# Kernel optimization log

Measured on AMD Instinct MI355X. Metric: run time of the kernel, lower is better.

Reference implementation:

```python
import jax, jax.numpy as jnp
import numpy as np
from jax import lax

B, N, C = 4, 4096, 512
NUM_HEADS = 8
HD = C // NUM_HEADS  # 64, equals L
L = 64               # H = W = L, N = L*L


def setup_inputs() -> dict:
    key = jax.random.key(0)
    ks = jax.random.split(key, 8)
    d = HD
    return {
        "x": jax.random.normal(ks[0], (B, N, C), jnp.float32),
        "log_peak_width": jnp.log(jnp.float32(3.0)),
        "log_valley_width": jnp.log(jnp.float32(3.0)),
        "w_qkv": jax.random.normal(ks[1], (3 * C, C), jnp.float32) * 0.02,
        "b_qkv": jnp.zeros((3 * C,), jnp.float32),
        "w_proj": jax.random.normal(ks[2], (C, C), jnp.float32) * 0.02,
        "b_proj": jnp.zeros((C,), jnp.float32),
        "omega": jnp.linspace(0.1, 10.0, d // 2).astype(jnp.float32),
        "w_pp1": jax.random.normal(ks[3], (2 * d, 1, 3), jnp.float32) * 0.3,   # grouped conv, groups=d
        "b_pp1": jnp.zeros((2 * d,), jnp.float32),
        "w_pp2": jax.random.normal(ks[4], (d, 2 * d, 1), jnp.float32) * 0.1,
        "b_pp2": jnp.zeros((d,), jnp.float32),
        "w_gate": jax.random.normal(ks[5], (d, d, 1), jnp.float32) * 0.1,
        "b_gate": jnp.zeros((d,), jnp.float32),
    }


def _spectral_gate(x_spec, log_pw, log_vw):
    # x_spec: [B, C, N]. torch nonzero flattens (b,c,i) -> use per-position counts
    # (exactly equivalent to summing one gaussian per nonzero occurrence).
    n = x_spec.shape[-1]
    sc = jnp.sign(jnp.diff(jnp.diff(x_spec, axis=-1), axis=-1))       # [B,C,N-2]
    peak_cnt = jnp.sum(sc < 0, axis=(0, 1)).astype(x_spec.dtype)      # [N-2]
    valley_cnt = jnp.sum(sc > 0, axis=(0, 1)).astype(x_spec.dtype)    # [N-2]
    pos = jnp.arange(n, dtype=x_spec.dtype)
    centers = jnp.arange(1, n - 1, dtype=x_spec.dtype)                # index i+1

    def gsum(cnt, logw):
        dist = (pos[None, :] - centers[:, None]) * jnp.exp(-logw)     # [N-2, N]
        return cnt @ jnp.exp(-dist * dist)                            # [N]

    attn = gsum(peak_cnt, log_pw) + gsum(valley_cnt, log_vw)
    return (attn - attn.min()) / (attn.max() - attn.min() + 1e-6)     # [N], uniform over (B,C)


def _spectral_pe(omega, w1, b1, w2, b2, wg, bg, l, d):
    grid = jnp.arange(l, dtype=jnp.float32)
    rel = grid[:, None] - grid[None, :]                               # [l,l]
    freqs = rel[..., None] * omega                                    # [l,l,d/2]
    pe = jnp.concatenate([jnp.sin(freqs), jnp.cos(freqs)], axis=-1)   # [l,l,d]
    pe = pe.reshape(l * l, d).T[None]                                 # [1,d,l*l]
    dn = ('NCH', 'OIH', 'NCH')
    h = lax.conv_general_dilated(pe, w1, (1,), [(1, 1)], dimension_numbers=dn,
                                 feature_group_count=d) + b1[None, :, None]
    h = jax.nn.gelu(h, approximate=False)
    pe2 = (lax.conv_general_dilated(h, w2, (1,), [(0, 0)],
                                    dimension_numbers=dn) + b2[None, :, None])[0]  # [d, l*l]
    gate = jax.nn.sigmoid(wg[:, :, 0] @ pe2.mean(-1, keepdims=True) + bg[:, None])  # [d,1]
    pe3 = pe2.T.reshape(l, l, d)
    # torch rearrange '(l1 l2) d -> l1 l2 d' on [d,1] gate: reshape to [l, d//l, 1] and broadcast
    return pe3 * gate.reshape(l, d // l, 1)


def _rope(t, pe, d):
    b, h, n, _ = t.shape
    l = pe.shape[0]
    tr = t.reshape(b, h, l, l, d)
    tr = tr + tr * pe * (d ** -0.25)
    return tr.reshape(b, h, n, d)


def reference(x, log_peak_width, log_valley_width, w_qkv, b_qkv, w_proj, b_proj,
              omega, w_pp1, b_pp1, w_pp2, b_pp2, w_gate, b_gate):
    b, n, c = x.shape
    h, d = NUM_HEADS, HD
    gate = _spectral_gate(x.transpose(0, 2, 1), log_peak_width, log_valley_width)  # [n]
    xg = x * gate[None, :, None]
    qkv = xg @ w_qkv.T + b_qkv                                        # [b,n,3c]
    q, k, v = jnp.split(qkv, 3, axis=-1)
    tohead = lambda t: t.reshape(b, n, h, d).transpose(0, 2, 1, 3)    # [b,h,n,d]
    q, k, v = tohead(q), tohead(k), tohead(v)
    q = jax.nn.elu(q) + 1.0
    k = jax.nn.elu(k) + 1.0
    pe = _spectral_pe(omega, w_pp1, b_pp1, w_pp2, b_pp2, w_gate, b_gate, L, d)
    q = _rope(q, pe, d)
    k = _rope(k, pe, d)
    scale = (d * n) ** -0.5
    ctx = jnp.einsum('bhnd,bhne->bhde', q, k) * scale                 # [b,h,d,d]
    out = jnp.einsum('bhnd,bhde->bhne', v, ctx) * scale               # [b,h,n,d]
    out = out.transpose(0, 2, 1, 3).reshape(b, n, c)
    return out @ w_proj.T + b_proj
```

## Files before the change

### kernel.cpp

```cpp
#include <hip/hip_runtime.h>
#include <hip/hip_bf16.h>
#include <math.h>

constexpr int BB = 4;
constexpr int NN = 4096;
constexpr int CC = 512;
constexpr int HH = 8;
constexpr int DD = 64;
constexpr int NCNT = NN - 2;

typedef __bf16 bf16x8 __attribute__((ext_vector_type(8)));
typedef float f32x4 __attribute__((ext_vector_type(4)));

__device__ __forceinline__ float b2f(ushort u) {
  unsigned v = ((unsigned)u) << 16;
  return __builtin_bit_cast(float, v);
}
__device__ __forceinline__ ushort f2b(float f) {
  __hip_bfloat16 h = __float2bfloat16(f);
  return __builtin_bit_cast(ushort, h);
}
__device__ __forceinline__ void gload16(const ushort* g, ushort* l) {
  __builtin_amdgcn_global_load_lds(
      (const __attribute__((address_space(1))) unsigned int*)g,
      (__attribute__((address_space(3))) unsigned int*)l, 16, 0, 0);
}

__global__ __launch_bounds__(512) void k_front(
    const float* __restrict__ x, int* __restrict__ pcntP,
    int* __restrict__ pcntV, ushort* __restrict__ Xh,
    const float* __restrict__ omega,
    const float* __restrict__ w1, const float* __restrict__ b1,
    const float* __restrict__ w2, const float* __restrict__ b2,
    float* __restrict__ pe2,
    const float* __restrict__ wqkv, ushort* __restrict__ Whqk,
    ushort* __restrict__ Wvth, ushort* __restrict__ Wvtl) {
  __shared__ __attribute__((aligned(16))) char sm[16896];
  const int blk = blockIdx.x;
  const int tid = threadIdx.x;

  if (blk < 1024) {
    int b = blk >> 8;
    int tile = blk & 255;
    int g = tid >> 7;
    int cq = tid & 127;
    int c4 = cq * 4;
    int lane = tid & 63;
    int r0 = tile * 16 + g * 4;
    const float* xb = x + (size_t)b * NN * CC + c4;

    float4 v[6];
    #pragma unroll
    for (int r = 0; r < 6; ++r) {
      int row = r0 + r;
      v[r] = *(const float4*)&xb[(size_t)(row < NN ? row : NN - 1) * CC];
    }

    #pragma unroll
    for (int r = 0; r < 4; ++r) {
      ushort4 h;
      ((ushort*)&h)[0] = f2b(v[r].x);
      ((ushort*)&h)[1] = f2b(v[r].y);
      ((ushort*)&h)[2] = f2b(v[r].z);
      ((ushort*)&h)[3] = f2b(v[r].w);
      *(ushort4*)&Xh[((size_t)b * NN + r0 + r) * CC + c4] = h;
    }

    unsigned* red = (unsigned*)sm;
    if (tid < 16) red[tid] = 0;
    __syncthreads();
    #pragma unroll
    for (int r = 0; r < 4; ++r) {
      int i = r0 + r;
      if (i < NCNT) {
        float d2x = (v[r + 2].x - v[r + 1].x) - (v[r + 1].x - v[r].x);
        float d2y = (v[r + 2].y - v[r + 1].y) - (v[r + 1].y - v[r].y);
        float d2z = (v[r + 2].z - v[r + 1].z) - (v[r + 1].z - v[r].z);
        float d2w = (v[r + 2].w - v[r + 1].w) - (v[r + 1].w - v[r].w);
        unsigned neg = (d2x < 0.f) + (d2y < 0.f) + (d2z < 0.f) + (d2w < 0.f);
        unsigned pos = (d2x > 0.f) + (d2y > 0.f) + (d2z > 0.f) + (d2w > 0.f);
        unsigned packed = neg | (pos << 16);
        #pragma unroll
        for (int off = 32; off > 0; off >>= 1)
          packed += __shfl_down(packed, off);
        if (lane == 0) atomicAdd(&red[g * 4 + r], packed);
      }
    }
    __syncthreads();
    if (tid < 16) {
      int i = tile * 16 + tid;
      unsigned p = red[tid];
      pcntP[b * NN + i] = (i < NCNT) ? (int)(p & 0xffffu) : 0;
      pcntV[b * NN + i] = (i < NCNT) ? (int)(p >> 16) : 0;
    }
  } else if (blk < 1536) {
    int pblk = blk - 1024;
    int g = tid >> 6;
    int j = tid & 63;
    int n = pblk * 8 + g;
    float (*pec)[3][64] = (float (*)[3][64])sm;
    float (*hs)[128] = (float (*)[128])(sm + 6144);
    for (int t = 0; t < 3; ++t) {
      int m = n + t - 1;
      float v = 0.f;
      if (m >= 0 && m < NN) {
        int l1 = m >> 6, l2 = m & 63;
        float rel = (float)(l1 - l2);
        v = (j < 32) ? sinf(rel * omega[j]) : cosf(rel * omega[j - 32]);
      }
      pec[g][t][j] = v;
    }
    __syncthreads();
    for (int o = j; o < 128; o += 64) {
      int ci = o >> 1;
      float hv = b1[o];
      #pragma unroll
      for (int t = 0; t < 3; ++t) hv += pec[g][t][ci] * w1[o * 3 + t];
      hv = 0.5f * hv * (1.f + erff(hv * 0.70710678118654752f));
      hs[g][o] = hv;
    }
    __syncthreads();
    float acc = b2[j];
    for (int o = 0; o < 128; ++o) acc += hs[g][o] * w2[j * 128 + o];
    pe2[(size_t)j * NN + n] = acc;
  } else if (blk < 1792) {
    int hblk = blk - 1536;
    int idx4 = (hblk * 512 + tid) * 4;
    float4 v = *(const float4*)&wqkv[idx4];
    ushort4 h;
    ((ushort*)&h)[0] = f2b(v.x);
    ((ushort*)&h)[1] = f2b(v.y);
    ((ushort*)&h)[2] = f2b(v.z);
    ((ushort*)&h)[3] = f2b(v.w);
    *(ushort4*)&Whqk[idx4] = h;
  } else {
    int wblk = blk - 1792;
    int bx = wblk & 7;
    int by = wblk >> 3;
    float (*t)[65] = (float (*)[65])sm;
    if (tid < 256) {
      #pragma unroll
      for (int it = 0; it < 4; ++it) {
        int idx = tid + it * 256;
        int r = idx >> 4;
        int c4 = (idx & 15) * 4;
        float4 v = *(const float4*)&wqkv[(size_t)(1024 + by * 64 + r) * 512 + bx * 64 + c4];
        t[r][c4] = v.x; t[r][c4 + 1] = v.y; t[r][c4 + 2] = v.z; t[r][c4 + 3] = v.w;
      }
    }
    __syncthreads();
    if (tid < 256) {
      #pragma unroll
      for (int it = 0; it < 4; ++it) {
        int idx = tid + it * 256;
        int r = idx >> 4;
        int c4 = (idx & 15) * 4;
        ushort4 h4, l4;
        #pragma unroll
        for (int q = 0; q < 4; ++q) {
          float v = t[c4 + q][r];
          ushort hi = f2b(v);
          ((ushort*)&h4)[q] = hi;
          ((ushort*)&l4)[q] = f2b(v - b2f(hi));
        }
        size_t o = (size_t)(bx * 64 + r) * 512 + by * 64 + c4;
        *(ushort4*)&Wvth[o] = h4;
        *(ushort4*)&Wvtl[o] = l4;
      }
    }
  }
}

__global__ __launch_bounds__(256) void k_mid1(
    const float* __restrict__ lpw, const float* __restrict__ lvw,
    const int* __restrict__ pcntP, const int* __restrict__ pcntV,
    float* __restrict__ etabP, float* __restrict__ etabV,
    float* __restrict__ fcntP, float* __restrict__ fcntV,
    const float* __restrict__ pe2, const float* __restrict__ wg,
    const float* __restrict__ bg, float* __restrict__ gpe) {
  const int blk = blockIdx.x;
  const int tid = threadIdx.x;
  if (blk < 16) {
    int i = blk * 256 + tid;
    float ipw = expf(-lpw[0]);
    float ivw = expf(-lvw[0]);
    float t1 = (float)i * ipw;
    float t2 = (float)i * ivw;
    etabP[i] = expf(-t1 * t1);
    etabV[i] = expf(-t2 * t2);
    fcntP[i] = (float)(pcntP[i] + pcntP[NN + i] + pcntP[2 * NN + i] + pcntP[3 * NN + i]);
    fcntV[i] = (float)(pcntV[i] + pcntV[NN + i] + pcntV[2 * NN + i] + pcntV[3 * NN + i]);
  } else {
    int j = tid & 63, part = tid >> 6;
    float s = 0.f;
    const float* row = pe2 + (size_t)j * NN + part * 1024;
    for (int t = 0; t < 1024; ++t) s += row[t];
    __shared__ float ps[4][64];
    __shared__ float mean[64];
    ps[part][j] = s;
    __syncthreads();
    if (tid < 64) mean[j] = (ps[0][j] + ps[1][j] + ps[2][j] + ps[3][j]) * (1.f / 4096.f);
    __syncthreads();
    if (tid < 64) {
      float g = bg[j];
      for (int k2 = 0; k2 < 64; ++k2) g += wg[j * 64 + k2] * mean[k2];
      gpe[j] = 1.f / (1.f + expf(-g));
    }
  }
}

__global__ __launch_bounds__(256) void k_mid2(
    const float* __restrict__ fcntP, const float* __restrict__ fcntV,
    const float* __restrict__ etabP, const float* __restrict__ etabV,
    float* __restrict__ attn,
    const float* __restrict__ pe2, const float* __restrict__ gpe,
    float* __restrict__ ropem) {
  const int blk = blockIdx.x;
  const int tid = threadIdx.x;
  if (blk < 4096) {
    int p = blk;
    float acc = 0.f;
    for (int i = tid; i < NCNT; i += 256) {
      int a = p - 1 - i;
      a = a < 0 ? -a : a;
      acc += fcntP[i] * etabP[a] + fcntV[i] * etabV[a];
    }
    __shared__ float red[256];
    red[tid] = acc;
    __syncthreads();
    for (int s = 128; s > 0; s >>= 1) {
      if (tid < s) red[tid] += red[tid + s];
      __syncthreads();
    }
    if (tid == 0) attn[p] = red[0];
  } else {
    int idx = (blk - 4096) * 256 + tid;
    int n = idx >> 6, dd = idx & 63;
    ropem[idx] = 1.f + pe2[(size_t)dd * NN + n] * gpe[n >> 6] * 0.35355339059327373f;
  }
}

__global__ void k_norm(const float* __restrict__ attn, float* __restrict__ gate) {
  int tid = threadIdx.x;
  float v0 = attn[tid], v1 = attn[tid + 1024], v2 = attn[tid + 2048], v3 = attn[tid + 3072];
  float mn = fminf(fminf(v0, v1), fminf(v2, v3));
  float mx = fmaxf(fmaxf(v0, v1), fmaxf(v2, v3));
  __shared__ float rmn[1024], rmx[1024];
  rmn[tid] = mn; rmx[tid] = mx;
  __syncthreads();
  for (int s = 512; s > 0; s >>= 1) {
    if (tid < s) {
      rmn[tid] = fminf(rmn[tid], rmn[tid + s]);
      rmx[tid] = fmaxf(rmx[tid], rmx[tid + s]);
    }
    __syncthreads();
  }
  float lo = rmn[0];
  float denom = rmx[0] - rmn[0] + 1e-6f;
  gate[tid]        = (v0 - lo) / denom;
  gate[tid + 1024] = (v1 - lo) / denom;
  gate[tid + 2048] = (v2 - lo) / denom;
  gate[tid + 3072] = (v3 - lo) / denom;
}

template <int BN, int EPI>
__global__ __launch_bounds__(512) void k_gemm8(
    const ushort* __restrict__ Ag, const ushort* __restrict__ Bgh,
    const float* __restrict__ bias, const float* __restrict__ gate,
    const float* __restrict__ ropem,
    float* __restrict__ outF, ushort* __restrict__ qT, ushort* __restrict__ kT,
    int ntn, int ncols) {
  constexpr int NF = BN / 32;
  constexpr int BCH = BN / 16;
  const int nwg = gridDim.x;
  const int hw = blockIdx.x;
  const int logical = (hw & 7) * (nwg >> 3) + (hw >> 3);
  const int m0 = (logical / ntn) * 256, n0 = (logical % ntn) * BN;

  const int tid = threadIdx.x, wave = tid >> 6, lane = tid & 63;
  const int wm = wave >> 1, wn = wave & 1;
  __shared__ ushort sA[2][8192];
  __shared__ ushort sB[2][BN * 32];
  f32x4 acc[4][NF] = {};

  const int lr = lane >> 2;
  const int ci = lane & 3;
  const int scol = (ci ^ ((lr >> 1) & 3)) * 8;
  const int rA = lane & 15;
  const int cswz = ((lane >> 4) ^ ((rA >> 1) & 3)) * 8;

  const ushort* pA0 = Ag + (size_t)(m0 + (2 * wave) * 16 + lr) * CC + scol;
  const ushort* pA1 = Ag + (size_t)(m0 + (2 * wave + 1) * 16 + lr) * CC + scol;
  const ushort* Bh_ = Bgh + (EPI == 2 ? (size_t)(m0 >> 12) * 262144 : 0);
  const ushort* pB0 = Bh_ + (size_t)(n0 + wave * 16 + lr) * CC + scol;

#define STAGE(T, S)                                                        \
  {                                                                        \
    gload16(pA0 + (T) * 32, &sA[S][(2 * wave) * 512]);                     \
    gload16(pA1 + (T) * 32, &sA[S][(2 * wave + 1) * 512]);                 \
    if (BCH == 8) {                                                        \
      gload16(pB0 + (T) * 32, &sB[S][wave * 512]);                         \
    } else {                                                               \
      if (wave < BCH) gload16(pB0 + (T) * 32, &sB[S][wave * 512]);         \
    }                                                                      \
  }

  STAGE(0, 0);
  __syncthreads();

  #pragma unroll
  for (int t = 0; t < 16; ++t) {
    if (t < 15) STAGE(t + 1, (t + 1) & 1);
    const int cur = t & 1;
    bf16x8 af[4], bhf[NF];
    #pragma unroll
    for (int m = 0; m < 4; ++m)
      af[m] = *(const bf16x8*)(&sA[cur][(wm * 64 + m * 16 + rA) * 32 + cswz]);
    #pragma unroll
    for (int n = 0; n < NF; ++n)
      bhf[n] = *(const bf16x8*)(&sB[cur][(wn * (BN / 2) + n * 16 + rA) * 32 + cswz]);
    #pragma unroll
    for (int m = 0; m < 4; ++m)
      #pragma unroll
      for (int n = 0; n < NF; ++n)
        acc[m][n] = __builtin_amdgcn_mfma_f32_16x16x32_bf16(af[m], bhf[n], acc[m][n], 0, 0, 0);
    __syncthreads();
  }
#undef STAGE

  const int kj = lane >> 4, l15 = lane & 15;
  #pragma unroll
  for (int m = 0; m < 4; ++m) {
    #pragma unroll
    for (int n = 0; n < NF; ++n) {
      if (EPI == 2) {
        #pragma unroll
        for (int r = 0; r < 4; ++r) {
          int row = m0 + wm * 64 + m * 16 + kj * 4 + r;
          int col = n0 + wn * (BN / 2) + n * 16 + l15;
          int nseq = row & (NN - 1), b = row >> 12;
          float val = acc[m][n][r] * gate[nseq] + bias[b * 512 + col];
          outF[(size_t)row * ncols + col] = val;
        }
      } else {
        int rowb = m0 + wm * 64 + m * 16 + kj * 4;
        int col = n0 + wn * (BN / 2) + n * 16 + l15;
        int nseqb = rowb & (NN - 1), b = rowb >> 12;
        int part = col >> 9, h = (col >> 6) & 7, dd = col & 63;
        ushort4 pk;
        #pragma unroll
        for (int r = 0; r < 4; ++r) {
          int nseq = nseqb + r;
          float val = acc[m][n][r] * gate[nseq] + bias[col];
          float e = val > 0.f ? val + 1.f : expf(val);
          ((ushort*)&pk)[r] = f2b(e * ropem[nseq * 64 + dd]);
        }
        ushort* dst = (part == 0 ? qT : kT) +
                      ((size_t)(b * HH + h) * DD + dd) * NN + nseqb;
        *(ushort4*)dst = pk;
      }
    }
  }
}

__global__ __launch_bounds__(256) void k_ctx_mfma(
    const ushort* __restrict__ qT, const ushort* __restrict__ kT,
    float* __restrict__ ctxp) {
  int blk = blockIdx.x;
  int bh = blk >> 4, chunk = blk & 15;
  int wave = threadIdx.x >> 6, lane = threadIdx.x & 63;
  int l15 = lane & 15, kj = lane >> 4;
  const size_t base = (size_t)bh * DD * NN;
  const int n0 = chunk * 256 + wave * 64;
  f32x4 acc[4][4] = {};
  #pragma unroll
  for (int ks = 0; ks < 2; ++ks) {
    const int nb = n0 + ks * 32 + kj * 8;
    bf16x8 qa[4], ka[4];
    #pragma unroll
    for (int m = 0; m < 4; ++m)
      qa[m] = *(const bf16x8*)(qT + base + (size_t)(m * 16 + l15) * NN + nb);
    #pragma unroll
    for (int n = 0; n < 4; ++n)
      ka[n] = *(const bf16x8*)(kT + base + (size_t)(n * 16 + l15) * NN + nb);
    #pragma unroll
    for (int m = 0; m < 4; ++m)
      #pragma unroll
      for (int n = 0; n < 4; ++n)
        acc[m][n] = __builtin_amdgcn_mfma_f32_16x16x32_bf16(qa[m], ka[n], acc[m][n], 0, 0, 0);
  }
  __shared__ float red[4][4096];
  #pragma unroll
  for (int m = 0; m < 4; ++m)
    #pragma unroll
    for (int n = 0; n < 4; ++n)
      #pragma unroll
      for (int r = 0; r < 4; ++r)
        red[wave][(m * 16 + kj * 4 + r) * 64 + n * 16 + l15] = acc[m][n][r];
  __syncthreads();
  const float scale = 1.f / 512.f;
  float* dst = ctxp + (size_t)(bh * 16 + chunk) * 4096;
  #pragma unroll
  for (int e = 0; e < 16; ++e) {
    int idx = threadIdx.x + e * 256;
    float s = red[0][idx] + red[1][idx] + red[2][idx] + red[3][idx];
    dst[idx] = s * scale;
  }
}

__global__ void k_ctx_red(const float* __restrict__ ctxp, float* __restrict__ ctx) {
  int idx = blockIdx.x * 256 + threadIdx.x;
  int bh = idx >> 12, off = idx & 4095;
  float s = 0.f;
  #pragma unroll
  for (int c2 = 0; c2 < 16; ++c2)
    s += ctxp[((size_t)bh * 16 + c2) * 4096 + off];
  ctx[idx] = s;
}

__global__ __launch_bounds__(256) void k_mproj(
    const float* __restrict__ ctx, const float* __restrict__ wp,
    ushort* __restrict__ Mfh, ushort* __restrict__ Mfl) {
  int blk = blockIdx.x;
  int b = blk >> 6, h = (blk >> 3) & 7, oq = blk & 7;
  int tid = threadIdx.x;
  int o = oq * 64 + (tid & 63);
  int d0 = (tid >> 6) * 16;
  __shared__ float cs[64][64];
  #pragma unroll
  for (int it = 0; it < 4; ++it) {
    int idx = (tid + 256 * it) * 4;
    *(float4*)&cs[idx >> 6][idx & 63] =
        *(const float4*)&ctx[(size_t)(b * 8 + h) * 4096 + idx];
  }
  __syncthreads();
  float wv[64];
  #pragma unroll
  for (int e = 0; e < 64; ++e) wv[e] = wp[(size_t)o * 512 + h * 64 + e];
  for (int d = d0; d < d0 + 16; ++d) {
    float s = 0.f;
    #pragma unroll
    for (int e = 0; e < 64; ++e) s += cs[d][e] * wv[e];
    s *= (1.f / 512.f);
    ushort hi = f2b(s);
    size_t idx = ((size_t)b * 512 + o) * 512 + h * 64 + d;
    Mfh[idx] = hi;
    Mfl[idx] = f2b(s - b2f(hi));
  }
}

__global__ __launch_bounds__(256) void k_tail(
    const ushort* __restrict__ Mfh, const ushort* __restrict__ Mfl,
    const ushort* __restrict__ Wvth, const ushort* __restrict__ Wvtl,
    ushort* __restrict__ G2h,
    const float* __restrict__ bqkv, const float* __restrict__ bproj,
    float* __restrict__ beff) {
  const int blk = blockIdx.x;
  if (blk < 64) {
    const int logical = (blk & 7) * 8 + (blk >> 3);
    const int m0 = (logical / 4) * 128, n0 = (logical % 4) * 128;
    const int tid = threadIdx.x, wave = tid >> 6, lane = tid & 63;
    const int wm = wave >> 1, wn = wave & 1;
    __shared__ ushort sA[2][4096];
    __shared__ ushort sB[2][8192];
    f32x4 acc[4][4] = {};

    const int lr = lane >> 2;
    const int ci = lane & 3;
    const int scol = (ci ^ ((lr >> 1) & 3)) * 8;
    const int rA = lane & 15;
    const int cswz = ((lane >> 4) ^ ((rA >> 1) & 3)) * 8;

    const int chunk0 = wave * 2, chunk1 = wave * 2 + 1;
    const ushort* pA0 = Mfh + (size_t)(m0 + chunk0 * 16 + lr) * CC + scol;
    const ushort* pA1 = Mfh + (size_t)(m0 + chunk1 * 16 + lr) * CC + scol;
    const ushort* pB0 = Wvth + (size_t)(n0 + chunk0 * 16 + lr) * CC + scol;
    const ushort* pB1 = Wvth + (size_t)(n0 + chunk1 * 16 + lr) * CC + scol;
    const ushort* pB0l = Wvtl + (size_t)(n0 + chunk0 * 16 + lr) * CC + scol;
    const ushort* pB1l = Wvtl + (size_t)(n0 + chunk1 * 16 + lr) * CC + scol;

#define STAGE(T, S)                                                        \
    {                                                                      \
      gload16(pA0 + (T) * 32, &sA[S][chunk0 * 512]);                       \
      gload16(pA1 + (T) * 32, &sA[S][chunk1 * 512]);                       \
      gload16(pB0 + (T) * 32, &sB[S][chunk0 * 512]);                       \
      gload16(pB1 + (T) * 32, &sB[S][chunk1 * 512]);                       \
      gload16(pB0l + (T) * 32, &sB[S][4096 + chunk0 * 512]);               \
      gload16(pB1l + (T) * 32, &sB[S][4096 + chunk1 * 512]);               \
    }

    STAGE(0, 0);
    __syncthreads();
    #pragma unroll
    for (int t = 0; t < 16; ++t) {
      if (t < 15) STAGE(t + 1, (t + 1) & 1);
      const int cur = t & 1;
      bf16x8 af[4], bh[4], bl[4];
      #pragma unroll
      for (int m = 0; m < 4; ++m)
        af[m] = *(const bf16x8*)(&sA[cur][(wm * 64 + m * 16 + rA) * 32 + cswz]);
      #pragma unroll
      for (int n = 0; n < 4; ++n) {
        int off = (wn * 64 + n * 16 + rA) * 32 + cswz;
        bh[n] = *(const bf16x8*)(&sB[cur][off]);
        bl[n] = *(const bf16x8*)(&sB[cur][4096 + off]);
      }
      #pragma unroll
      for (int m = 0; m < 4; ++m)
        #pragma unroll
        for (int n = 0; n < 4; ++n) {
          acc[m][n] = __builtin_amdgcn_mfma_f32_16x16x32_bf16(af[m], bh[n], acc[m][n], 0, 0, 0);
          acc[m][n] = __builtin_amdgcn_mfma_f32_16x16x32_bf16(af[m], bl[n], acc[m][n], 0, 0, 0);
        }
      __syncthreads();
    }
#undef STAGE

    const int kj = lane >> 4, l15 = lane & 15;
    #pragma unroll
    for (int m = 0; m < 4; ++m)
      #pragma unroll
      for (int n = 0; n < 4; ++n)
        #pragma unroll
        for (int r = 0; r < 4; ++r) {
          int row = m0 + wm * 64 + m * 16 + kj * 4 + r;
          int col = n0 + wn * 64 + n * 16 + l15;
          G2h[(size_t)row * 512 + col] = f2b(acc[m][n][r]);
        }
  } else {
    int w = threadIdx.x >> 6, lane = threadIdx.x & 63;
    int t = (blk - 64) * 4 + w;
    int b = t >> 9, o = t & 511;
    size_t base = ((size_t)b * 512 + o) * 512;
    float s = 0.f;
    #pragma unroll
    for (int c = 0; c < 512; c += 64) {
      float m = b2f(Mfh[base + c + lane]) + b2f(Mfl[base + c + lane]);
      s += bqkv[1024 + c + lane] * m;
    }
    #pragma unroll
    for (int off = 32; off > 0; off >>= 1) s += __shfl_down(s, off);
    if (lane == 0) beff[t] = s + bproj[o];
  }
}

extern "C" void kernel_launch(void* const* d_in, const int* in_sizes, int n_in,
                              void* d_out, int out_size, void* d_ws, size_t ws_size,
                              hipStream_t stream) {
  const float* x    = (const float*)d_in[0];
  const float* lpw  = (const float*)d_in[1];
  const float* lvw  = (const float*)d_in[2];
  const float* wqkv = (const float*)d_in[3];
  const float* bqkv = (const float*)d_in[4];
  const float* wproj= (const float*)d_in[5];
  const float* bproj= (const float*)d_in[6];
  const float* omega= (const float*)d_in[7];
  const float* w1   = (const float*)d_in[8];
  const float* b1   = (const float*)d_in[9];
  const float* w2   = (const float*)d_in[10];
  const float* b2   = (const float*)d_in[11];
  const float* wg   = (const float*)d_in[12];
  const float* bg   = (const float*)d_in[13];
  float* out = (float*)d_out;

  constexpr size_t MB = 1024 * 1024;
  char* w = (char*)d_ws;
  int*   pcntP  = (int*)(w);
  int*   pcntV  = (int*)(w + 64 * 1024);
  float* attn   = (float*)(w + 128 * 1024);
  float* gate   = (float*)(w + 144 * 1024);
  float* etabP  = (float*)(w + 160 * 1024);
  float* etabV  = (float*)(w + 176 * 1024);
  float* fcntP  = (float*)(w + 192 * 1024);
  float* fcntV  = (float*)(w + 208 * 1024);
  float* pe2    = (float*)(w + 256 * 1024);
  float* gpe    = (float*)(w + 1280 * 1024);
  float* ropem  = (float*)(w + 1344 * 1024);
  ushort* Xh    = (ushort*)(w + 4 * MB);
  ushort* qT    = (ushort*)(w + 20 * MB);
  ushort* kT    = (ushort*)(w + 36 * MB);
  ushort* Whqk  = (ushort*)(w + 52 * MB);
  ushort* Wvth  = (ushort*)(w + 53 * MB);
  ushort* Wvtl  = (ushort*)(w + 53 * MB + 512 * 1024);
  ushort* Mfh   = (ushort*)(w + 54 * MB);
  ushort* Mfl   = (ushort*)(w + 56 * MB);
  ushort* G2h   = (ushort*)(w + 58 * MB);
  float* beff   = (float*)(w + 60 * MB);
  float* ctxp   = (float*)(w + 61 * MB);
  float* ctx    = (float*)(w + 69 * MB);

  k_front<<<1856, 512, 0, stream>>>(x, pcntP, pcntV, Xh, omega, w1, b1, w2, b2,
                                    pe2, wqkv, Whqk, Wvth, Wvtl);
  k_mid1<<<17, 256, 0, stream>>>(lpw, lvw, pcntP, pcntV, etabP, etabV,
                                 fcntP, fcntV, pe2, wg, bg, gpe);
  k_mid2<<<5120, 256, 0, stream>>>(fcntP, fcntV, etabP, etabV, attn,
                                   pe2, gpe, ropem);
  k_norm<<<1, 1024, 0, stream>>>(attn, gate);

  k_gemm8<128, 1><<<512, 512, 0, stream>>>(Xh, Whqk, bqkv, gate, ropem,
                                           nullptr, qT, kT, 8, 0);
  k_ctx_mfma<<<512, 256, 0, stream>>>(qT, kT, ctxp);
  k_ctx_red<<<512, 256, 0, stream>>>(ctxp, ctx);
  k_mproj<<<256, 256, 0, stream>>>(ctx, wproj, Mfh, Mfl);
  k_tail<<<576, 256, 0, stream>>>(Mfh, Mfl, Wvth, Wvtl, G2h, bqkv, bproj, beff);

  k_gemm8<64, 2><<<512, 512, 0, stream>>>(Xh, G2h, beff, gate, nullptr,
                                          out, nullptr, nullptr, 8, 512);
}
```

Before: 170.4 us.

## Triple-buffer A tiles with explicit vmcnt waits in GEMM main loop

```diff
diff --git a/kernel.cpp b/kernel.cpp
--- a/kernel.cpp
+++ b/kernel.cpp
@@ -279,7 +279,7 @@
 
   const int tid = threadIdx.x, wave = tid >> 6, lane = tid & 63;
   const int wm = wave >> 1, wn = wave & 1;
-  __shared__ ushort sA[2][8192];
+  __shared__ ushort sA[3][8192];
   __shared__ ushort sB[2][BN * 32];
   f32x4 acc[4][NF] = {};
 
@@ -294,10 +294,13 @@
   const ushort* Bh_ = Bgh + (EPI == 2 ? (size_t)(m0 >> 12) * 262144 : 0);
   const ushort* pB0 = Bh_ + (size_t)(n0 + wave * 16 + lr) * CC + scol;
 
-#define STAGE(T, S)                                                        \
+#define STAGEA(T, S)                                                       \
   {                                                                        \
     gload16(pA0 + (T) * 32, &sA[S][(2 * wave) * 512]);                     \
     gload16(pA1 + (T) * 32, &sA[S][(2 * wave + 1) * 512]);                 \
+  }
+#define STAGEB(T, S)                                                       \
+  {                                                                        \
     if (BCH == 8) {                                                        \
       gload16(pB0 + (T) * 32, &sB[S][wave * 512]);                         \
     } else {                                                               \
@@ -305,28 +308,44 @@
     }                                                                      \
   }
 
-  STAGE(0, 0);
-  __syncthreads();
+  STAGEB(0, 0);
+  STAGEA(0, 0);
+  STAGEA(1, 1);
+  asm volatile("s_waitcnt vmcnt(2)" ::: "memory");
+  __builtin_amdgcn_sched_barrier(0);
+  __builtin_amdgcn_s_barrier();
+  __builtin_amdgcn_sched_barrier(0);
 
   #pragma unroll
   for (int t = 0; t < 16; ++t) {
-    if (t < 15) STAGE(t + 1, (t + 1) & 1);
-    const int cur = t & 1;
+    if (t + 1 < 16) STAGEB(t + 1, (t + 1) & 1);
+    if (t + 2 < 16) STAGEA(t + 2, (t + 2) % 3);
+    const int curA = t % 3, curB = t & 1;
     bf16x8 af[4], bhf[NF];
     #pragma unroll
     for (int m = 0; m < 4; ++m)
-      af[m] = *(const bf16x8*)(&sA[cur][(wm * 64 + m * 16 + rA) * 32 + cswz]);
+      af[m] = *(const bf16x8*)(&sA[curA][(wm * 64 + m * 16 + rA) * 32 + cswz]);
     #pragma unroll
     for (int n = 0; n < NF; ++n)
-      bhf[n] = *(const bf16x8*)(&sB[cur][(wn * (BN / 2) + n * 16 + rA) * 32 + cswz]);
+      bhf[n] = *(const bf16x8*)(&sB[curB][(wn * (BN / 2) + n * 16 + rA) * 32 + cswz]);
     #pragma unroll
     for (int m = 0; m < 4; ++m)
       #pragma unroll
       for (int n = 0; n < NF; ++n)
         acc[m][n] = __builtin_amdgcn_mfma_f32_16x16x32_bf16(af[m], bhf[n], acc[m][n], 0, 0, 0);
-    __syncthreads();
-  }
-#undef STAGE
+    if (t < 15) {
+      if (t < 14) {
+        asm volatile("s_waitcnt vmcnt(2)" ::: "memory");
+      } else {
+        asm volatile("s_waitcnt vmcnt(0)" ::: "memory");
+      }
+      __builtin_amdgcn_sched_barrier(0);
+      __builtin_amdgcn_s_barrier();
+      __builtin_amdgcn_sched_barrier(0);
+    }
+  }
+#undef STAGEA
+#undef STAGEB
 
   const int kj = lane >> 4, l15 = lane & 15;
   #pragma unroll
```

New measurement: 176.9 us. 1.04x slower.
